# Performance work log

Measured on AMD Instinct MI355X. Metric: run time of the kernel, lower is better.

Reference implementation:

```python
import jax, jax.numpy as jnp
import numpy as np

D_MODEL, D_STATE, D_CONV, EXPAND = 1024, 16, 4, 2
D_INNER = EXPAND * D_MODEL
BATCH, L = 2, 2048


def setup_inputs() -> dict:
    key = jax.random.key(0)
    ks = jax.random.split(key, 8)
    s = lambda fan: 1.0 / float(np.sqrt(fan))
    x = jax.random.normal(ks[0], (BATCH, L, D_MODEL), jnp.float32)
    W_in = jax.random.normal(ks[1], (D_MODEL, 2 * D_INNER), jnp.float32) * s(D_MODEL)
    conv_w = jax.random.normal(ks[2], (D_INNER, 1, D_CONV), jnp.float32) * s(D_CONV)
    conv_b = jax.random.normal(ks[3], (D_INNER,), jnp.float32) * 0.1
    W_x = jax.random.normal(ks[4], (D_INNER, 2 * D_STATE + 1), jnp.float32) * s(D_INNER)
    w_dt = jax.random.normal(ks[5], (D_INNER,), jnp.float32)
    b_dt = jax.random.normal(ks[6], (D_INNER,), jnp.float32) * 0.1
    W_out = jax.random.normal(ks[7], (D_INNER, D_MODEL), jnp.float32) * s(D_INNER)
    A_log = jnp.log(jnp.broadcast_to(jnp.arange(1, D_STATE + 1, dtype=jnp.float32), (D_INNER, D_STATE)))
    Dp = jnp.ones((D_INNER,), jnp.float32)
    return dict(x=x, W_in=W_in, conv_w=conv_w, conv_b=conv_b, W_x=W_x,
                w_dt=w_dt, b_dt=b_dt, A_log=A_log, Dp=Dp, W_out=W_out)


def _silu(v):
    return v * jax.nn.sigmoid(v)


def _forward(x, W_in, conv_w, conv_b, W_x, w_dt, b_dt, A_log, Dp, W_out):
    xz = x @ W_in                                   # (B,L,2*Di)
    x_, z = jnp.split(xz, 2, axis=-1)               # (B,L,Di) each
    # causal depthwise conv over length (== torch pad d_conv-1 both sides then [:L])
    xc = jnp.transpose(x_, (0, 2, 1))               # (B,Di,L)
    xc = jax.lax.conv_general_dilated(
        xc, conv_w, window_strides=(1,), padding=[(D_CONV - 1, 0)],
        dimension_numbers=('NCH', 'OIH', 'NCH'), feature_group_count=D_INNER)
    xc = xc + conv_b[None, :, None]
    x_ = _silu(jnp.transpose(xc, (0, 2, 1)))        # (B,L,Di)

    bcd = x_ @ W_x                                  # (B,L,2N+1)
    B_ = bcd[..., :D_STATE]                         # (B,L,N)
    C = bcd[..., D_STATE:2 * D_STATE]               # (B,L,N)
    dt = jax.nn.softplus(bcd[..., -1:] * w_dt + b_dt)  # (B,L,Di)
    A = -jnp.exp(A_log)                             # (Di,N)

    def step(h, inp):
        dt_t, B_t, C_t, x_t = inp                   # (B,Di),(B,N),(B,N),(B,Di)
        dA = jnp.exp(dt_t[..., None] * A)           # (B,Di,N)
        h = dA * h + (dt_t * x_t)[..., None] * B_t[:, None, :]
        y = jnp.einsum('bdn,bn->bd', h, C_t)
        return h, y

    h0 = jnp.zeros((x.shape[0], D_INNER, D_STATE), x.dtype)
    xs = (jnp.transpose(dt, (1, 0, 2)), jnp.transpose(B_, (1, 0, 2)),
          jnp.transpose(C, (1, 0, 2)), jnp.transpose(x_, (1, 0, 2)))
    _, ys = jax.lax.scan(step, h0, xs)              # ys: (L,B,Di)
    y = jnp.transpose(ys, (1, 0, 2)) + x_ * Dp      # skip connection via D
    return (y * _silu(z)) @ W_out                   # (B,L,d_model)


def reference(x, W_in, conv_w, conv_b, W_x, w_dt, b_dt, A_log, Dp, W_out):
    return _forward(x, W_in, conv_w, conv_b, W_x, w_dt, b_dt, A_log, Dp, W_out)
```

## Files before the change

kernel.cpp:

```cpp
#include <hip/hip_runtime.h>
#include <hip/hip_bf16.h>
#include <stdint.h>

#define D_MODEL 1024
#define D_STATE 16
#define D_CONV  4
#define D_INNER 2048
#define BATCH   2
#define SEQLEN  2048
#define NROWS   (BATCH*SEQLEN)
#define BCD_LD  36
#define NCHUNK  64
#define CHUNKLEN (SEQLEN/NCHUNK)
#define KS2     16
#define L2E 1.44269504088896340f

typedef __attribute__((ext_vector_type(8))) short   short8;
typedef __attribute__((ext_vector_type(4))) float   f32x4;

__device__ __forceinline__ uint16_t f2bf(float f) {
    uint32_t u = __float_as_uint(f);
    return (uint16_t)((u + 0x7FFFu + ((u >> 16) & 1u)) >> 16);
}
__device__ __forceinline__ uint32_t pack2bf(float lo, float hi) {
    return (uint32_t)f2bf(lo) | ((uint32_t)f2bf(hi) << 16);
}
__device__ __forceinline__ void gload16(const uint16_t* g, uint16_t* l) {
    __builtin_amdgcn_global_load_lds(
        (const __attribute__((address_space(1))) void*)g,
        (__attribute__((address_space(3))) void*)l, 16, 0, 0);
}
__device__ __forceinline__ void gload16f(const float* g, float* l) {
    __builtin_amdgcn_global_load_lds(
        (const __attribute__((address_space(1))) void*)g,
        (__attribute__((address_space(3))) void*)l, 16, 0, 0);
}
__device__ __forceinline__ float softplus_f(float v) {
    return fmaxf(v, 0.f) + __logf(1.f + __expf(-fabsf(v)));
}
__device__ __forceinline__ float silu_f(float v) {
    return v / (1.f + __expf(-v));
}
__device__ __forceinline__ short8 pack8(const float4 lo, const float4 hi) {
    short8 r;
    r[0] = (short)f2bf(lo.x); r[1] = (short)f2bf(lo.y);
    r[2] = (short)f2bf(lo.z); r[3] = (short)f2bf(lo.w);
    r[4] = (short)f2bf(hi.x); r[5] = (short)f2bf(hi.y);
    r[6] = (short)f2bf(hi.z); r[7] = (short)f2bf(hi.w);
    return r;
}

__global__ void kcvt(const float* __restrict__ in, uint16_t* __restrict__ out, int n4) {
    int T = blockIdx.x * 256 + threadIdx.x;
    if (T >= n4) return;
    const float4 v = *(const float4*)&in[(size_t)T * 4];
    ushort4 o;
    o.x = f2bf(v.x); o.y = f2bf(v.y); o.z = f2bf(v.z); o.w = f2bf(v.w);
    *(ushort4*)&out[(size_t)T * 4] = o;
}

__global__ void ktrans(const float* __restrict__ in, uint16_t* __restrict__ out,
                       int Kd, int Nd) {
    __shared__ float tile[32][33];
    const int n0 = blockIdx.x * 32, k0 = blockIdx.y * 32;
    const int tx = threadIdx.x & 31, ty = threadIdx.x >> 5;
#pragma unroll
    for (int i = 0; i < 4; ++i)
        tile[ty + i * 8][tx] = in[(size_t)(k0 + ty + i * 8) * Nd + n0 + tx];
    __syncthreads();
#pragma unroll
    for (int i = 0; i < 4; ++i)
        out[(size_t)(n0 + ty + i * 8) * Kd + k0 + tx] = f2bf(tile[tx][ty + i * 8]);
}

__global__ void kwxt(const float* __restrict__ Wx, float* __restrict__ Wxt) {
    const int T = blockIdx.x * 256 + threadIdx.x;
    const int j = T >> 11, k = T & 2047;
    Wxt[T] = (j < 33) ? Wx[(size_t)k * 33 + j] : 0.f;
}

template<int KDIM, int GXL>
__global__ __launch_bounds__(256) void kgemm(const uint16_t* __restrict__ A,
                                             const uint16_t* __restrict__ B,
                                             float* __restrict__ C, const int ldc) {
    __shared__ uint16_t As[128 * 32];
    __shared__ uint16_t Bs[128 * 32];
    const int t = threadIdx.x;
    const int w = t >> 6, lane = t & 63;
    int wg = blockIdx.y * (1 << GXL) + blockIdx.x;
    wg = (wg & 7) * ((gridDim.x * gridDim.y) >> 3) + (wg >> 3);
    const int m0 = (wg >> GXL) * 128, n0 = (wg & ((1 << GXL) - 1)) * 128;
    const int wm = (w >> 1) * 64, wn = (w & 1) * 64;
    f32x4 acc[4][4] = {};

    const int srow = t >> 2;
    const int scol = ((t & 3) ^ ((t >> 3) & 3)) * 8;
    const uint16_t* ga0 = A + (size_t)(m0 + srow) * KDIM + scol;
    const uint16_t* ga1 = A + (size_t)(m0 + 64 + srow) * KDIM + scol;
    const uint16_t* gb0 = B + (size_t)(n0 + srow) * KDIM + scol;
    const uint16_t* gb1 = B + (size_t)(n0 + 64 + srow) * KDIM + scol;
    uint16_t* lA0 = &As[w * 512];
    uint16_t* lA1 = &As[2048 + w * 512];
    uint16_t* lB0 = &Bs[w * 512];
    uint16_t* lB1 = &Bs[2048 + w * 512];

    const int fr = lane & 15, fg = (lane >> 4) * 8;
    const int psl = (((fg >> 3) ^ ((fr >> 1) & 3)) << 3);

    for (int kt = 0; kt < KDIM / 32; ++kt) {
        const int ko = kt * 32;
        gload16(ga0 + ko, lA0);
        gload16(ga1 + ko, lA1);
        gload16(gb0 + ko, lB0);
        gload16(gb1 + ko, lB1);
        __syncthreads();
        short8 a[4], b[4];
#pragma unroll
        for (int i = 0; i < 4; ++i) {
            a[i] = *(const short8*)&As[(wm + i * 16 + fr) * 32 + psl];
            b[i] = *(const short8*)&Bs[(wn + i * 16 + fr) * 32 + psl];
        }
#pragma unroll
        for (int i = 0; i < 4; ++i)
#pragma unroll
            for (int j = 0; j < 4; ++j)
                acc[i][j] = __builtin_amdgcn_mfma_f32_16x16x32_bf16(a[i], b[j], acc[i][j], 0, 0, 0);
        __syncthreads();
    }
    const int cr = (lane >> 4) * 4, cc = lane & 15;
#pragma unroll
    for (int i = 0; i < 4; ++i)
#pragma unroll
        for (int j = 0; j < 4; ++j)
#pragma unroll
            for (int r = 0; r < 4; ++r)
                C[(size_t)(m0 + wm + i * 16 + cr + r) * ldc + (n0 + wn + j * 16 + cc)] = acc[i][j][r];
}

template<int KDIM, int GXL>
__global__ __launch_bounds__(256) void kgemm64(const uint16_t* __restrict__ A,
                                               const uint16_t* __restrict__ B,
                                               float* __restrict__ C, const int ldc) {
    __shared__ uint16_t As[64 * 32];
    __shared__ uint16_t Bs[128 * 32];
    const int t = threadIdx.x;
    const int w = t >> 6, lane = t & 63;
    int wg = blockIdx.y * (1 << GXL) + blockIdx.x;
    wg = (wg & 7) * ((gridDim.x * gridDim.y) >> 3) + (wg >> 3);
    const int m0 = (wg >> GXL) * 64, n0 = (wg & ((1 << GXL) - 1)) * 128;
    const int wm = (w >> 1) * 32, wn = (w & 1) * 64;
    f32x4 acc[2][4] = {};

    const int srow = t >> 2;
    const int scol = ((t & 3) ^ ((t >> 3) & 3)) * 8;
    const uint16_t* ga0 = A + (size_t)(m0 + srow) * KDIM + scol;
    const uint16_t* gb0 = B + (size_t)(n0 + srow) * KDIM + scol;
    const uint16_t* gb1 = B + (size_t)(n0 + 64 + srow) * KDIM + scol;
    uint16_t* lA0 = &As[w * 512];
    uint16_t* lB0 = &Bs[w * 512];
    uint16_t* lB1 = &Bs[2048 + w * 512];

    const int fr = lane & 15, fg = (lane >> 4) * 8;
    const int psl = (((fg >> 3) ^ ((fr >> 1) & 3)) << 3);

    for (int kt = 0; kt < KDIM / 32; ++kt) {
        const int ko = kt * 32;
        gload16(ga0 + ko, lA0);
        gload16(gb0 + ko, lB0);
        gload16(gb1 + ko, lB1);
        __syncthreads();
        short8 a[2], b[4];
#pragma unroll
        for (int i = 0; i < 2; ++i)
            a[i] = *(const short8*)&As[(wm + i * 16 + fr) * 32 + psl];
#pragma unroll
        for (int j = 0; j < 4; ++j)
            b[j] = *(const short8*)&Bs[(wn + j * 16 + fr) * 32 + psl];
#pragma unroll
        for (int i = 0; i < 2; ++i)
#pragma unroll
            for (int j = 0; j < 4; ++j)
                acc[i][j] = __builtin_amdgcn_mfma_f32_16x16x32_bf16(a[i], b[j], acc[i][j], 0, 0, 0);
        __syncthreads();
    }
    const int cr = (lane >> 4) * 4, cc = lane & 15;
#pragma unroll
    for (int i = 0; i < 2; ++i)
#pragma unroll
        for (int j = 0; j < 4; ++j)
#pragma unroll
            for (int r = 0; r < 4; ++r)
                C[(size_t)(m0 + wm + i * 16 + cr + r) * ldc + (n0 + wn + j * 16 + cc)] = acc[i][j][r];
}

__global__ __launch_bounds__(256) void kgemm2m(const float* __restrict__ xs,
        const float* __restrict__ Wxt, float* __restrict__ part) {
    __shared__ float As[128 * 32];
    __shared__ float Bs[64 * 32];
    const int t = threadIdx.x;
    const int w = t >> 6, lane = t & 63;
    const int kb = blockIdx.x;
    const int m0 = blockIdx.y * 128;
    const int kc = kb * 128;
    f32x4 acc[2][3] = {};

    const int srow = t >> 3;
    const int scol = ((t & 7) ^ ((t >> 3) & 7)) * 4;
    float* lA[4]; float* lB[2];
#pragma unroll
    for (int r = 0; r < 4; ++r) lA[r] = &As[(r * 32 + w * 8) * 32];
#pragma unroll
    for (int r = 0; r < 2; ++r) lB[r] = &Bs[(r * 32 + w * 8) * 32];

    const int wm = w * 32;
    const int fr = lane & 15, fg = (lane >> 4) * 8;
    const int plo = (((fg >> 2) ^ (fr & 7))) * 4;
    const int phi = ((((fg >> 2) + 1) ^ (fr & 7))) * 4;

    for (int kt = 0; kt < 4; ++kt) {
        const int ko = kc + kt * 32;
#pragma unroll
        for (int r = 0; r < 4; ++r)
            gload16f(xs + (size_t)(m0 + r * 32 + srow) * 2048 + ko + scol, lA[r]);
#pragma unroll
        for (int r = 0; r < 2; ++r)
            gload16f(Wxt + (size_t)(r * 32 + srow) * 2048 + ko + scol, lB[r]);
        __syncthreads();
        short8 a[2], b[3];
#pragma unroll
        for (int i = 0; i < 2; ++i) {
            const float* base = &As[(wm + i * 16 + fr) * 32];
            a[i] = pack8(*(const float4*)&base[plo], *(const float4*)&base[phi]);
        }
#pragma unroll
        for (int j = 0; j < 3; ++j) {
            const float* base = &Bs[(j * 16 + fr) * 32];
            b[j] = pack8(*(const float4*)&base[plo], *(const float4*)&base[phi]);
        }
#pragma unroll
        for (int i = 0; i < 2; ++i)
#pragma unroll
            for (int j = 0; j < 3; ++j)
                acc[i][j] = __builtin_amdgcn_mfma_f32_16x16x32_bf16(a[i], b[j], acc[i][j], 0, 0, 0);
        __syncthreads();
    }
    const int cr = (lane >> 4) * 4, cc = lane & 15;
    float* pb = part + (size_t)kb * 4096 * 48;
#pragma unroll
    for (int i = 0; i < 2; ++i)
#pragma unroll
        for (int j = 0; j < 3; ++j)
#pragma unroll
            for (int r = 0; r < 4; ++r)
                pb[(size_t)(m0 + wm + i * 16 + cr + r) * 48 + j * 16 + cc] = acc[i][j][r];
}

__global__ void kred2(const float* __restrict__ part, float* __restrict__ bcd) {
    const int T = blockIdx.x * 256 + threadIdx.x;
    if (T >= 4096 * 48) return;
    const int row = T / 48, j = T - row * 48;
    if (j >= 33) return;
    float s = 0.f;
#pragma unroll
    for (int ks = 0; ks < KS2; ++ks) s += part[(size_t)ks * 4096 * 48 + T];
    bcd[(size_t)row * BCD_LD + j] = s;
}

__global__ void kprep(const float* __restrict__ bcd, const float* __restrict__ wdt,
                      const float* __restrict__ bdt, const float* __restrict__ Dp,
                      const float* __restrict__ xs, float* __restrict__ xz) {
    const int T = blockIdx.x * 256 + threadIdx.x;
    const int row = T >> 9, dg = (T & 511) * 4;
    const float raw = bcd[(size_t)row * BCD_LD + 32];
    const float4 w  = *(const float4*)&wdt[dg];
    const float4 b  = *(const float4*)&bdt[dg];
    const float4 Dv = *(const float4*)&Dp[dg];
    const float4 xv = *(const float4*)&xs[(size_t)row * D_INNER + dg];
    const float4 zv = *(const float4*)&xz[(size_t)row * 4096 + 2048 + dg];
    const float dt0 = softplus_f(raw * w.x + b.x);
    const float dt1 = softplus_f(raw * w.y + b.y);
    const float dt2 = softplus_f(raw * w.z + b.z);
    const float dt3 = softplus_f(raw * w.w + b.w);
    uint4 pd, ps;
    pd.x = pack2bf(dt0, dt0 * xv.x);
    pd.y = pack2bf(dt1, dt1 * xv.y);
    pd.z = pack2bf(dt2, dt2 * xv.z);
    pd.w = pack2bf(dt3, dt3 * xv.w);
    const float s0 = silu_f(zv.x), s1 = silu_f(zv.y), s2 = silu_f(zv.z), s3 = silu_f(zv.w);
    ps.x = pack2bf(s0, xv.x * Dv.x * s0);
    ps.y = pack2bf(s1, xv.y * Dv.y * s1);
    ps.z = pack2bf(s2, xv.z * Dv.z * s2);
    ps.w = pack2bf(s3, xv.w * Dv.w * s3);
    uint32_t* xzu = (uint32_t*)xz;
    *(uint4*)&xzu[(size_t)row * 4096 + dg] = pd;
    *(uint4*)&xzu[(size_t)row * 4096 + 2048 + dg] = ps;
}

__global__ __launch_bounds__(256) void kscan1(const uint32_t* __restrict__ dtdx,
        const float* __restrict__ bcd, const float* __restrict__ Alog,
        float* __restrict__ hbuf, float* __restrict__ sumdt) {
    const int T = blockIdx.x * 256 + threadIdx.x;
    const int sub = T & 1;
    const int ch  = (T >> 1) & 4095;
    const int chunk = T >> 13;
    const int b = ch >> 11, d = ch & 2047;
    float Ae[8]; bool st = true;
#pragma unroll
    for (int i = 0; i < 8; ++i) {
        const float a = __expf(Alog[d * 16 + sub * 8 + i]);
        Ae[i] = -a * L2E;
        st = st && (fabsf(a - (float)(sub * 8 + i + 1)) < 1e-3f);
    }
    float h[8] = {};
    float sdt = 0.f;
    const int row0 = b * SEQLEN + chunk * CHUNKLEN;
    const uint32_t* pD = dtdx + (size_t)row0 * 4096 + d;
    const float* pB = bcd + (size_t)row0 * BCD_LD + sub * 8;
    if (st) {
        for (int l0 = 0; l0 < CHUNKLEN; l0 += 2) {
            uint32_t pk[2]; float4 B0[2], B1[2];
#pragma unroll
            for (int s = 0; s < 2; ++s) {
                pk[s] = pD[(size_t)s * 4096];
                B0[s] = *(const float4*)(pB + s * BCD_LD);
                B1[s] = *(const float4*)(pB + s * BCD_LD + 4);
            }
#pragma unroll
            for (int s = 0; s < 2; ++s) {
                const float dt  = __uint_as_float(pk[s] << 16);
                const float dtx = __uint_as_float(pk[s] & 0xffff0000u);
                sdt += dt;
                const float e0 = __builtin_amdgcn_exp2f(dt * (-L2E));
                const float e2 = e0 * e0, e4 = e2 * e2, e8 = e4 * e4;
                float dec = sub ? e8 : 1.f;
                dec *= e0; h[0] = fmaf(dec, h[0], dtx * B0[s].x);
                dec *= e0; h[1] = fmaf(dec, h[1], dtx * B0[s].y);
                dec *= e0; h[2] = fmaf(dec, h[2], dtx * B0[s].z);
                dec *= e0; h[3] = fmaf(dec, h[3], dtx * B0[s].w);
                dec *= e0; h[4] = fmaf(dec, h[4], dtx * B1[s].x);
                dec *= e0; h[5] = fmaf(dec, h[5], dtx * B1[s].y);
                dec *= e0; h[6] = fmaf(dec, h[6], dtx * B1[s].z);
                dec *= e0; h[7] = fmaf(dec, h[7], dtx * B1[s].w);
            }
            pD += 2 * 4096; pB += 2 * BCD_LD;
        }
    } else {
        for (int l0 = 0; l0 < CHUNKLEN; l0 += 2) {
            uint32_t pk[2]; float4 B0[2], B1[2];
#pragma unroll
            for (int s = 0; s < 2; ++s) {
                pk[s] = pD[(size_t)s * 4096];
                B0[s] = *(const float4*)(pB + s * BCD_LD);
                B1[s] = *(const float4*)(pB + s * BCD_LD + 4);
            }
#pragma unroll
            for (int s = 0; s < 2; ++s) {
                const float dt  = __uint_as_float(pk[s] << 16);
                const float dtx = __uint_as_float(pk[s] & 0xffff0000u);
                sdt += dt;
                h[0] = fmaf(__builtin_amdgcn_exp2f(dt * Ae[0]), h[0], dtx * B0[s].x);
                h[1] = fmaf(__builtin_amdgcn_exp2f(dt * Ae[1]), h[1], dtx * B0[s].y);
                h[2] = fmaf(__builtin_amdgcn_exp2f(dt * Ae[2]), h[2], dtx * B0[s].z);
                h[3] = fmaf(__builtin_amdgcn_exp2f(dt * Ae[3]), h[3], dtx * B0[s].w);
                h[4] = fmaf(__builtin_amdgcn_exp2f(dt * Ae[4]), h[4], dtx * B1[s].x);
                h[5] = fmaf(__builtin_amdgcn_exp2f(dt * Ae[5]), h[5], dtx * B1[s].y);
                h[6] = fmaf(__builtin_amdgcn_exp2f(dt * Ae[6]), h[6], dtx * B1[s].z);
                h[7] = fmaf(__builtin_amdgcn_exp2f(dt * Ae[7]), h[7], dtx * B1[s].w);
            }
            pD += 2 * 4096; pB += 2 * BCD_LD;
        }
    }
    const size_t cc = (size_t)(chunk * 4096 + ch) * 16 + sub * 8;
    *(float4*)&hbuf[cc]     = make_float4(h[0], h[1], h[2], h[3]);
    *(float4*)&hbuf[cc + 4] = make_float4(h[4], h[5], h[6], h[7]);
    if (sub == 0) sumdt[chunk * 4096 + ch] = sdt;
}

__global__ void kscan2(float* __restrict__ hbuf, const float* __restrict__ sumdt,
                       const float* __restrict__ Alog) {
    const int T = blockIdx.x * 256 + threadIdx.x;
    const int n = T & 15, ch = T >> 4;
    const int d = ch & 2047;
    const float Ae = -__expf(Alog[d * 16 + n]) * L2E;
    float h = 0.f;
    for (int c = 0; c < NCHUNK; ++c) {
        const size_t idx = (size_t)(c * 4096 + ch) * 16 + n;
        const float loc = hbuf[idx];
        hbuf[idx] = h;
        h = __builtin_amdgcn_exp2f(Ae * sumdt[c * 4096 + ch]) * h + loc;
    }
}

__global__ __launch_bounds__(256) void kscan3(const uint32_t* __restrict__ dtdx,
        const float* __restrict__ bcd, const float* __restrict__ Alog,
        const uint32_t* __restrict__ szw, const float* __restrict__ hbuf,
        uint16_t* __restrict__ u) {
    const int T = blockIdx.x * 256 + threadIdx.x;
    const int sub = T & 1;
    const int ch  = (T >> 1) & 4095;
    const int chunk = T >> 13;
    const int b = ch >> 11, d = ch & 2047;
    float Ae[8]; bool st = true;
#pragma unroll
    for (int i = 0; i < 8; ++i) {
        const float a = __expf(Alog[d * 16 + sub * 8 + i]);
        Ae[i] = -a * L2E;
        st = st && (fabsf(a - (float)(sub * 8 + i + 1)) < 1e-3f);
    }
    float h[8];
    {
        const size_t cc = (size_t)(chunk * 4096 + ch) * 16 + sub * 8;
        const float4 h0 = *(const float4*)&hbuf[cc];
        const float4 h1 = *(const float4*)&hbuf[cc + 4];
        h[0] = h0.x; h[1] = h0.y; h[2] = h0.z; h[3] = h0.w;
        h[4] = h1.x; h[5] = h1.y; h[6] = h1.z; h[7] = h1.w;
    }
    const int row0 = b * SEQLEN + chunk * CHUNKLEN;
    const uint32_t* pD = dtdx + (size_t)row0 * 4096 + d;
    const uint32_t* pS = szw  + (size_t)row0 * 4096 + d;
    const float* pB = bcd + (size_t)row0 * BCD_LD + sub * 8;
    uint16_t* pU = u + (size_t)row0 * D_INNER + d;
    if (st) {
        for (int l0 = 0; l0 < CHUNKLEN; l0 += 2) {
            uint32_t pk[2], qk[2]; float4 B0[2], B1[2], C0[2], C1[2];
#pragma unroll
            for (int s = 0; s < 2; ++s) {
                pk[s] = pD[(size_t)s * 4096];
                B0[s] = *(const float4*)(pB + s * BCD_LD);
                B1[s] = *(const float4*)(pB + s * BCD_LD + 4);
                C0[s] = *(const float4*)(pB + s * BCD_LD + 16);
                C1[s] = *(const float4*)(pB + s * BCD_LD + 20);
                if (sub == 0) qk[s] = pS[(size_t)s * 4096];
            }
#pragma unroll
            for (int s = 0; s < 2; ++s) {
                const float dt  = __uint_as_float(pk[s] << 16);
                const float dtx = __uint_as_float(pk[s] & 0xffff0000u);
                const float e0 = __builtin_amdgcn_exp2f(dt * (-L2E));
                const float e2 = e0 * e0, e4 = e2 * e2, e8 = e4 * e4;
                float dec = sub ? e8 : 1.f;
                dec *= e0; h[0] = fmaf(dec, h[0], dtx * B0[s].x);
                dec *= e0; h[1] = fmaf(dec, h[1], dtx * B0[s].y);
                dec *= e0; h[2] = fmaf(dec, h[2], dtx * B0[s].z);
                dec *= e0; h[3] = fmaf(dec, h[3], dtx * B0[s].w);
                dec *= e0; h[4] = fmaf(dec, h[4], dtx * B1[s].x);
                dec *= e0; h[5] = fmaf(dec, h[5], dtx * B1[s].y);
                dec *= e0; h[6] = fmaf(dec, h[6], dtx * B1[s].z);
                dec *= e0; h[7] = fmaf(dec, h[7], dtx * B1[s].w);
                float y = h[0] * C0[s].x + h[1] * C0[s].y + h[2] * C0[s].z + h[3] * C0[s].w
                        + h[4] * C1[s].x + h[5] * C1[s].y + h[6] * C1[s].z + h[7] * C1[s].w;
                y += __shfl_xor(y, 1);
                if (sub == 0) {
                    const float sz = __uint_as_float(qk[s] << 16);
                    const float w2 = __uint_as_float(qk[s] & 0xffff0000u);
                    pU[(size_t)s * D_INNER] = f2bf(fmaf(y, sz, w2));
                }
            }
            pD += 2 * 4096; pS += 2 * 4096; pB += 2 * BCD_LD; pU += 2 * D_INNER;
        }
    } else {
        for (int l0 = 0; l0 < CHUNKLEN; l0 += 2) {
            uint32_t pk[2], qk[2]; float4 B0[2], B1[2], C0[2], C1[2];
#pragma unroll
            for (int s = 0; s < 2; ++s) {
                pk[s] = pD[(size_t)s * 4096];
                B0[s] = *(const float4*)(pB + s * BCD_LD);
                B1[s] = *(const float4*)(pB + s * BCD_LD + 4);
                C0[s] = *(const float4*)(pB + s * BCD_LD + 16);
                C1[s] = *(const float4*)(pB + s * BCD_LD + 20);
                if (sub == 0) qk[s] = pS[(size_t)s * 4096];
            }
#pragma unroll
            for (int s = 0; s < 2; ++s) {
                const float dt  = __uint_as_float(pk[s] << 16);
                const float dtx = __uint_as_float(pk[s] & 0xffff0000u);
                h[0] = fmaf(__builtin_amdgcn_exp2f(dt * Ae[0]), h[0], dtx * B0[s].x);
                h[1] = fmaf(__builtin_amdgcn_exp2f(dt * Ae[1]), h[1], dtx * B0[s].y);
                h[2] = fmaf(__builtin_amdgcn_exp2f(dt * Ae[2]), h[2], dtx * B0[s].z);
                h[3] = fmaf(__builtin_amdgcn_exp2f(dt * Ae[3]), h[3], dtx * B0[s].w);
                h[4] = fmaf(__builtin_amdgcn_exp2f(dt * Ae[4]), h[4], dtx * B1[s].x);
                h[5] = fmaf(__builtin_amdgcn_exp2f(dt * Ae[5]), h[5], dtx * B1[s].y);
                h[6] = fmaf(__builtin_amdgcn_exp2f(dt * Ae[6]), h[6], dtx * B1[s].z);
                h[7] = fmaf(__builtin_amdgcn_exp2f(dt * Ae[7]), h[7], dtx * B1[s].w);
                float y = h[0] * C0[s].x + h[1] * C0[s].y + h[2] * C0[s].z + h[3] * C0[s].w
                        + h[4] * C1[s].x + h[5] * C1[s].y + h[6] * C1[s].z + h[7] * C1[s].w;
                y += __shfl_xor(y, 1);
                if (sub == 0) {
                    const float sz = __uint_as_float(qk[s] << 16);
                    const float w2 = __uint_as_float(qk[s] & 0xffff0000u);
                    pU[(size_t)s * D_INNER] = f2bf(fmaf(y, sz, w2));
                }
            }
            pD += 2 * 4096; pS += 2 * 4096; pB += 2 * BCD_LD; pU += 2 * D_INNER;
        }
    }
}

__global__ void kconv(const float* __restrict__ xz, const float* __restrict__ cw,
                      const float* __restrict__ cb, float* __restrict__ xs) {
    size_t T = (size_t)blockIdx.x * 256 + threadIdx.x;
    int d = (int)(T & (D_INNER - 1));
    int row = (int)(T >> 11);
    int l = row & (SEQLEN - 1), b = row >> 11;
    const float4 w4 = *(const float4*)&cw[d * 4];
    float acc = cb[d];
    const size_t base = (size_t)b * SEQLEN;
    if (l >= 3) {
        acc += w4.x * xz[(base + l - 3) * 4096 + d];
        acc += w4.y * xz[(base + l - 2) * 4096 + d];
        acc += w4.z * xz[(base + l - 1) * 4096 + d];
        acc += w4.w * xz[(base + l    ) * 4096 + d];
    } else {
        if (l >= 2) acc += w4.y * xz[(base + l - 2) * 4096 + d];
        if (l >= 1) acc += w4.z * xz[(base + l - 1) * 4096 + d];
        acc += w4.w * xz[(base + l) * 4096 + d];
    }
    xs[T] = silu_f(acc);
}

extern "C" void kernel_launch(void* const* d_in, const int* in_sizes, int n_in,
                              void* d_out, int out_size, void* d_ws, size_t ws_size,
                              hipStream_t stream) {
    const float* x      = (const float*)d_in[0];
    const float* W_in   = (const float*)d_in[1];
    const float* conv_w = (const float*)d_in[2];
    const float* conv_b = (const float*)d_in[3];
    const float* W_x    = (const float*)d_in[4];
    const float* w_dt   = (const float*)d_in[5];
    const float* b_dt   = (const float*)d_in[6];
    const float* A_log  = (const float*)d_in[7];
    const float* Dp     = (const float*)d_in[8];
    const float* W_out  = (const float*)d_in[9];
    float* out = (float*)d_out;

    char* p = (char*)d_ws;
    uint16_t* xb  = (uint16_t*)p;  p += (size_t)NROWS * D_MODEL * 2;
    uint16_t* Wb  = (uint16_t*)p;  p += (size_t)4096 * 1024 * 2;
    uint16_t* Wob = (uint16_t*)p;  p += (size_t)1024 * 2048 * 2;
    float* xz     = (float*)p;     p += (size_t)NROWS * 4096 * 4;
    float* xs     = (float*)p;     p += (size_t)NROWS * D_INNER * 4;
    float* bcd    = (float*)p;     p += (size_t)NROWS * BCD_LD * 4;
    float* sumdt  = (float*)p;     p += (size_t)NCHUNK * 4096 * 4;
    float* Wxt    = (float*)p;     p += (size_t)64 * 2048 * 4;
    uint16_t* ub  = (uint16_t*)p;  p += (size_t)NROWS * D_INNER * 2;
    float* hbuf   = (float*)xb;
    float* part   = (float*)ub;
    uint32_t* dtdx = (uint32_t*)xz;
    uint32_t* szw  = (uint32_t*)xz + 2048;

    kcvt<<<(NROWS * D_MODEL / 4 + 255) / 256, 256, 0, stream>>>(x, xb, NROWS * D_MODEL / 4);
    ktrans<<<dim3(4096 / 32, 1024 / 32), 256, 0, stream>>>(W_in, Wb, 1024, 4096);
    ktrans<<<dim3(1024 / 32, 2048 / 32), 256, 0, stream>>>(W_out, Wob, 2048, 1024);
    kwxt<<<(64 * 2048) / 256, 256, 0, stream>>>(W_x, Wxt);
    kgemm<1024, 5><<<dim3(32, 32), 256, 0, stream>>>(xb, Wb, xz, 4096);
    kconv<<<NROWS * D_INNER / 256, 256, 0, stream>>>(xz, conv_w, conv_b, xs);
    kgemm2m<<<dim3(KS2, 32), 256, 0, stream>>>(xs, Wxt, part);
    kred2<<<(4096 * 48 + 255) / 256, 256, 0, stream>>>(part, bcd);
    kprep<<<(4096 * 512) / 256, 256, 0, stream>>>(bcd, w_dt, b_dt, Dp, xs, xz);
    kscan1<<<(4096 * 2 * NCHUNK) / 256, 256, 0, stream>>>(dtdx, bcd, A_log, hbuf, sumdt);
    kscan2<<<(4096 * 16) / 256, 256, 0, stream>>>(hbuf, sumdt, A_log);
    kscan3<<<(4096 * 2 * NCHUNK) / 256, 256, 0, stream>>>(dtdx, bcd, A_log, szw, hbuf, ub);
    kgemm64<2048, 3><<<dim3(1024 / 128, 4096 / 64), 256, 0, stream>>>(ub, Wob, out, 1024);
}
```

Measured before the change: 240.8 us.

## Store in-projection output as bf16 and enlarge GEMM tile to 256x128

The in-projection GEMM now writes bf16 instead of fp32, halving the bytes written by the GEMM and read by the conv and prep kernels. The GEMM tile grows to 256x128 with 512 threads (8 waves) for more reuse of the B operand per block. The packed dt/dt*x data is written in place over xs and the silu(z) data goes to a separate buffer, so the scan kernels read with a row stride of 2048 instead of 4096. Storing the intermediate in bf16 adds rounding error, and the larger blocks use more registers and LDS, which may lower occupancy.

```diff
diff --git a/kernel.cpp b/kernel.cpp
--- a/kernel.cpp
+++ b/kernel.cpp
@@ -22,6 +22,9 @@
     uint32_t u = __float_as_uint(f);
     return (uint16_t)((u + 0x7FFFu + ((u >> 16) & 1u)) >> 16);
 }
+__device__ __forceinline__ float bf2f(uint16_t h) {
+    return __uint_as_float(((uint32_t)h) << 16);
+}
 __device__ __forceinline__ uint32_t pack2bf(float lo, float hi) {
     return (uint32_t)f2bf(lo) | ((uint32_t)f2bf(hi) << 16);
 }
@@ -80,29 +83,27 @@
 }
 
 template<int KDIM, int GXL>
-__global__ __launch_bounds__(256) void kgemm(const uint16_t* __restrict__ A,
-                                             const uint16_t* __restrict__ B,
-                                             float* __restrict__ C, const int ldc) {
-    __shared__ uint16_t As[128 * 32];
+__global__ __launch_bounds__(512) void kgemm256(const uint16_t* __restrict__ A,
+                                                const uint16_t* __restrict__ B,
+                                                uint16_t* __restrict__ C, const int ldc) {
+    __shared__ uint16_t As[256 * 32];
     __shared__ uint16_t Bs[128 * 32];
     const int t = threadIdx.x;
     const int w = t >> 6, lane = t & 63;
     int wg = blockIdx.y * (1 << GXL) + blockIdx.x;
     wg = (wg & 7) * ((gridDim.x * gridDim.y) >> 3) + (wg >> 3);
-    const int m0 = (wg >> GXL) * 128, n0 = (wg & ((1 << GXL) - 1)) * 128;
+    const int m0 = (wg >> GXL) * 256, n0 = (wg & ((1 << GXL) - 1)) * 128;
     const int wm = (w >> 1) * 64, wn = (w & 1) * 64;
     f32x4 acc[4][4] = {};
 
     const int srow = t >> 2;
     const int scol = ((t & 3) ^ ((t >> 3) & 3)) * 8;
     const uint16_t* ga0 = A + (size_t)(m0 + srow) * KDIM + scol;
-    const uint16_t* ga1 = A + (size_t)(m0 + 64 + srow) * KDIM + scol;
+    const uint16_t* ga1 = A + (size_t)(m0 + 128 + srow) * KDIM + scol;
     const uint16_t* gb0 = B + (size_t)(n0 + srow) * KDIM + scol;
-    const uint16_t* gb1 = B + (size_t)(n0 + 64 + srow) * KDIM + scol;
     uint16_t* lA0 = &As[w * 512];
-    uint16_t* lA1 = &As[2048 + w * 512];
+    uint16_t* lA1 = &As[4096 + w * 512];
     uint16_t* lB0 = &Bs[w * 512];
-    uint16_t* lB1 = &Bs[2048 + w * 512];
 
     const int fr = lane & 15, fg = (lane >> 4) * 8;
     const int psl = (((fg >> 3) ^ ((fr >> 1) & 3)) << 3);
@@ -112,7 +113,6 @@
         gload16(ga0 + ko, lA0);
         gload16(ga1 + ko, lA1);
         gload16(gb0 + ko, lB0);
-        gload16(gb1 + ko, lB1);
         __syncthreads();
         short8 a[4], b[4];
 #pragma unroll
@@ -134,7 +134,8 @@
         for (int j = 0; j < 4; ++j)
 #pragma unroll
             for (int r = 0; r < 4; ++r)
-                C[(size_t)(m0 + wm + i * 16 + cr + r) * ldc + (n0 + wn + j * 16 + cc)] = acc[i][j][r];
+                C[(size_t)(m0 + wm + i * 16 + cr + r) * ldc + (n0 + wn + j * 16 + cc)] =
+                    f2bf(acc[i][j][r]);
 }
 
 template<int KDIM, int GXL>
@@ -268,32 +269,34 @@
 
 __global__ void kprep(const float* __restrict__ bcd, const float* __restrict__ wdt,
                       const float* __restrict__ bdt, const float* __restrict__ Dp,
-                      const float* __restrict__ xs, float* __restrict__ xz) {
+                      float* __restrict__ xs_io, const uint16_t* __restrict__ xzb,
+                      uint32_t* __restrict__ szw) {
     const int T = blockIdx.x * 256 + threadIdx.x;
     const int row = T >> 9, dg = (T & 511) * 4;
     const float raw = bcd[(size_t)row * BCD_LD + 32];
     const float4 w  = *(const float4*)&wdt[dg];
     const float4 b  = *(const float4*)&bdt[dg];
     const float4 Dv = *(const float4*)&Dp[dg];
-    const float4 xv = *(const float4*)&xs[(size_t)row * D_INNER + dg];
-    const float4 zv = *(const float4*)&xz[(size_t)row * 4096 + 2048 + dg];
+    const float4 xv = *(const float4*)&xs_io[(size_t)row * 2048 + dg];
+    const ushort4 zu = *(const ushort4*)&xzb[(size_t)row * 4096 + 2048 + dg];
     const float dt0 = softplus_f(raw * w.x + b.x);
     const float dt1 = softplus_f(raw * w.y + b.y);
     const float dt2 = softplus_f(raw * w.z + b.z);
     const float dt3 = softplus_f(raw * w.w + b.w);
-    uint4 pd, ps;
-    pd.x = pack2bf(dt0, dt0 * xv.x);
-    pd.y = pack2bf(dt1, dt1 * xv.y);
-    pd.z = pack2bf(dt2, dt2 * xv.z);
-    pd.w = pack2bf(dt3, dt3 * xv.w);
-    const float s0 = silu_f(zv.x), s1 = silu_f(zv.y), s2 = silu_f(zv.z), s3 = silu_f(zv.w);
+    float4 pd;
+    pd.x = __uint_as_float(pack2bf(dt0, dt0 * xv.x));
+    pd.y = __uint_as_float(pack2bf(dt1, dt1 * xv.y));
+    pd.z = __uint_as_float(pack2bf(dt2, dt2 * xv.z));
+    pd.w = __uint_as_float(pack2bf(dt3, dt3 * xv.w));
+    const float s0 = silu_f(bf2f(zu.x)), s1 = silu_f(bf2f(zu.y));
+    const float s2 = silu_f(bf2f(zu.z)), s3 = silu_f(bf2f(zu.w));
+    uint4 ps;
     ps.x = pack2bf(s0, xv.x * Dv.x * s0);
     ps.y = pack2bf(s1, xv.y * Dv.y * s1);
     ps.z = pack2bf(s2, xv.z * Dv.z * s2);
     ps.w = pack2bf(s3, xv.w * Dv.w * s3);
-    uint32_t* xzu = (uint32_t*)xz;
-    *(uint4*)&xzu[(size_t)row * 4096 + dg] = pd;
-    *(uint4*)&xzu[(size_t)row * 4096 + 2048 + dg] = ps;
+    *(float4*)&xs_io[(size_t)row * 2048 + dg] = pd;
+    *(uint4*)&szw[(size_t)row * 2048 + dg] = ps;
 }
 
 __global__ __launch_bounds__(256) void kscan1(const uint32_t* __restrict__ dtdx,
@@ -314,14 +317,14 @@
     float h[8] = {};
     float sdt = 0.f;
     const int row0 = b * SEQLEN + chunk * CHUNKLEN;
-    const uint32_t* pD = dtdx + (size_t)row0 * 4096 + d;
+    const uint32_t* pD = dtdx + (size_t)row0 * 2048 + d;
     const float* pB = bcd + (size_t)row0 * BCD_LD + sub * 8;
     if (st) {
         for (int l0 = 0; l0 < CHUNKLEN; l0 += 2) {
             uint32_t pk[2]; float4 B0[2], B1[2];
 #pragma unroll
             for (int s = 0; s < 2; ++s) {
-                pk[s] = pD[(size_t)s * 4096];
+                pk[s] = pD[(size_t)s * 2048];
                 B0[s] = *(const float4*)(pB + s * BCD_LD);
                 B1[s] = *(const float4*)(pB + s * BCD_LD + 4);
             }
@@ -342,14 +345,14 @@
                 dec *= e0; h[6] = fmaf(dec, h[6], dtx * B1[s].z);
                 dec *= e0; h[7] = fmaf(dec, h[7], dtx * B1[s].w);
             }
-            pD += 2 * 4096; pB += 2 * BCD_LD;
+            pD += 2 * 2048; pB += 2 * BCD_LD;
         }
     } else {
         for (int l0 = 0; l0 < CHUNKLEN; l0 += 2) {
             uint32_t pk[2]; float4 B0[2], B1[2];
 #pragma unroll
             for (int s = 0; s < 2; ++s) {
-                pk[s] = pD[(size_t)s * 4096];
+                pk[s] = pD[(size_t)s * 2048];
                 B0[s] = *(const float4*)(pB + s * BCD_LD);
                 B1[s] = *(const float4*)(pB + s * BCD_LD + 4);
             }
@@ -367,7 +370,7 @@
                 h[6] = fmaf(__builtin_amdgcn_exp2f(dt * Ae[6]), h[6], dtx * B1[s].z);
                 h[7] = fmaf(__builtin_amdgcn_exp2f(dt * Ae[7]), h[7], dtx * B1[s].w);
             }
-            pD += 2 * 4096; pB += 2 * BCD_LD;
+            pD += 2 * 2048; pB += 2 * BCD_LD;
         }
     }
     const size_t cc = (size_t)(chunk * 4096 + ch) * 16 + sub * 8;
@@ -416,8 +419,8 @@
         h[4] = h1.x; h[5] = h1.y; h[6] = h1.z; h[7] = h1.w;
     }
     const int row0 = b * SEQLEN + chunk * CHUNKLEN;
-    const uint32_t* pD = dtdx + (size_t)row0 * 4096 + d;
-    const uint32_t* pS = szw  + (size_t)row0 * 4096 + d;
+    const uint32_t* pD = dtdx + (size_t)row0 * 2048 + d;
+    const uint32_t* pS = szw  + (size_t)row0 * 2048 + d;
     const float* pB = bcd + (size_t)row0 * BCD_LD + sub * 8;
     uint16_t* pU = u + (size_t)row0 * D_INNER + d;
     if (st) {
@@ -425,12 +428,12 @@
             uint32_t pk[2], qk[2]; float4 B0[2], B1[2], C0[2], C1[2];
 #pragma unroll
             for (int s = 0; s < 2; ++s) {
-                pk[s] = pD[(size_t)s * 4096];
+                pk[s] = pD[(size_t)s * 2048];
                 B0[s] = *(const float4*)(pB + s * BCD_LD);
                 B1[s] = *(const float4*)(pB + s * BCD_LD + 4);
                 C0[s] = *(const float4*)(pB + s * BCD_LD + 16);
                 C1[s] = *(const float4*)(pB + s * BCD_LD + 20);
-                if (sub == 0) qk[s] = pS[(size_t)s * 4096];
+                if (sub == 0) qk[s] = pS[(size_t)s * 2048];
             }
 #pragma unroll
             for (int s = 0; s < 2; ++s) {
@@ -456,19 +459,19 @@
                     pU[(size_t)s * D_INNER] = f2bf(fmaf(y, sz, w2));
                 }
             }
-            pD += 2 * 4096; pS += 2 * 4096; pB += 2 * BCD_LD; pU += 2 * D_INNER;
+            pD += 2 * 2048; pS += 2 * 2048; pB += 2 * BCD_LD; pU += 2 * D_INNER;
         }
     } else {
         for (int l0 = 0; l0 < CHUNKLEN; l0 += 2) {
             uint32_t pk[2], qk[2]; float4 B0[2], B1[2], C0[2], C1[2];
 #pragma unroll
             for (int s = 0; s < 2; ++s) {
-                pk[s] = pD[(size_t)s * 4096];
+                pk[s] = pD[(size_t)s * 2048];
                 B0[s] = *(const float4*)(pB + s * BCD_LD);
                 B1[s] = *(const float4*)(pB + s * BCD_LD + 4);
                 C0[s] = *(const float4*)(pB + s * BCD_LD + 16);
                 C1[s] = *(const float4*)(pB + s * BCD_LD + 20);
-                if (sub == 0) qk[s] = pS[(size_t)s * 4096];
+                if (sub == 0) qk[s] = pS[(size_t)s * 2048];
             }
 #pragma unroll
             for (int s = 0; s < 2; ++s) {
@@ -491,12 +494,12 @@
                     pU[(size_t)s * D_INNER] = f2bf(fmaf(y, sz, w2));
                 }
             }
-            pD += 2 * 4096; pS += 2 * 4096; pB += 2 * BCD_LD; pU += 2 * D_INNER;
-        }
-    }
-}
-
-__global__ void kconv(const float* __restrict__ xz, const float* __restrict__ cw,
+            pD += 2 * 2048; pS += 2 * 2048; pB += 2 * BCD_LD; pU += 2 * D_INNER;
+        }
+    }
+}
+
+__global__ void kconv(const uint16_t* __restrict__ xzb, const float* __restrict__ cw,
                       const float* __restrict__ cb, float* __restrict__ xs) {
     size_t T = (size_t)blockIdx.x * 256 + threadIdx.x;
     int d = (int)(T & (D_INNER - 1));
@@ -506,14 +509,14 @@
     float acc = cb[d];
     const size_t base = (size_t)b * SEQLEN;
     if (l >= 3) {
-        acc += w4.x * xz[(base + l - 3) * 4096 + d];
-        acc += w4.y * xz[(base + l - 2) * 4096 + d];
-        acc += w4.z * xz[(base + l - 1) * 4096 + d];
-        acc += w4.w * xz[(base + l    ) * 4096 + d];
+        acc += w4.x * bf2f(xzb[(base + l - 3) * 4096 + d]);
+        acc += w4.y * bf2f(xzb[(base + l - 2) * 4096 + d]);
+        acc += w4.z * bf2f(xzb[(base + l - 1) * 4096 + d]);
+        acc += w4.w * bf2f(xzb[(base + l    ) * 4096 + d]);
     } else {
-        if (l >= 2) acc += w4.y * xz[(base + l - 2) * 4096 + d];
-        if (l >= 1) acc += w4.z * xz[(base + l - 1) * 4096 + d];
-        acc += w4.w * xz[(base + l) * 4096 + d];
+        if (l >= 2) acc += w4.y * bf2f(xzb[(base + l - 2) * 4096 + d]);
+        if (l >= 1) acc += w4.z * bf2f(xzb[(base + l - 1) * 4096 + d]);
+        acc += w4.w * bf2f(xzb[(base + l) * 4096 + d]);
     }
     xs[T] = silu_f(acc);
 }
@@ -537,26 +540,26 @@
     uint16_t* xb  = (uint16_t*)p;  p += (size_t)NROWS * D_MODEL * 2;
     uint16_t* Wb  = (uint16_t*)p;  p += (size_t)4096 * 1024 * 2;
     uint16_t* Wob = (uint16_t*)p;  p += (size_t)1024 * 2048 * 2;
-    float* xz     = (float*)p;     p += (size_t)NROWS * 4096 * 4;
+    uint16_t* xzb = (uint16_t*)p;  p += (size_t)NROWS * 4096 * 2;
     float* xs     = (float*)p;     p += (size_t)NROWS * D_INNER * 4;
     float* bcd    = (float*)p;     p += (size_t)NROWS * BCD_LD * 4;
     float* sumdt  = (float*)p;     p += (size_t)NCHUNK * 4096 * 4;
     float* Wxt    = (float*)p;     p += (size_t)64 * 2048 * 4;
     uint16_t* ub  = (uint16_t*)p;  p += (size_t)NROWS * D_INNER * 2;
+    uint32_t* szw = (uint32_t*)p;  p += (size_t)NROWS * D_INNER * 4;
     float* hbuf   = (float*)xb;
     float* part   = (float*)ub;
-    uint32_t* dtdx = (uint32_t*)xz;
-    uint32_t* szw  = (uint32_t*)xz + 2048;
+    uint32_t* dtdx = (uint32_t*)xs;
 
     kcvt<<<(NROWS * D_MODEL / 4 + 255) / 256, 256, 0, stream>>>(x, xb, NROWS * D_MODEL / 4);
     ktrans<<<dim3(4096 / 32, 1024 / 32), 256, 0, stream>>>(W_in, Wb, 1024, 4096);
     ktrans<<<dim3(1024 / 32, 2048 / 32), 256, 0, stream>>>(W_out, Wob, 2048, 1024);
     kwxt<<<(64 * 2048) / 256, 256, 0, stream>>>(W_x, Wxt);
-    kgemm<1024, 5><<<dim3(32, 32), 256, 0, stream>>>(xb, Wb, xz, 4096);
-    kconv<<<NROWS * D_INNER / 256, 256, 0, stream>>>(xz, conv_w, conv_b, xs);
+    kgemm256<1024, 5><<<dim3(32, 16), 512, 0, stream>>>(xb, Wb, xzb, 4096);
+    kconv<<<NROWS * D_INNER / 256, 256, 0, stream>>>(xzb, conv_w, conv_b, xs);
     kgemm2m<<<dim3(KS2, 32), 256, 0, stream>>>(xs, Wxt, part);
     kred2<<<(4096 * 48 + 255) / 256, 256, 0, stream>>>(part, bcd);
-    kprep<<<(4096 * 512) / 256, 256, 0, stream>>>(bcd, w_dt, b_dt, Dp, xs, xz);
+    kprep<<<(4096 * 512) / 256, 256, 0, stream>>>(bcd, w_dt, b_dt, Dp, xs, xzb, szw);
     kscan1<<<(4096 * 2 * NCHUNK) / 256, 256, 0, stream>>>(dtdx, bcd, A_log, hbuf, sumdt);
     kscan2<<<(4096 * 16) / 256, 256, 0, stream>>>(hbuf, sumdt, A_log);
     kscan3<<<(4096 * 2 * NCHUNK) / 256, 256, 0, stream>>>(dtdx, bcd, A_log, szw, hbuf, ub);
```

New measurement: 223.4 us. 1.08x faster.
